# Optimization experiments

Measured on AMD Instinct MI355X. Metric: run time of the kernel, lower is better.

## Reference

```python
import jax, jax.numpy as jnp
import numpy as np

N, E = 25000, 400000
S, V, L2, T = 64, 32, 16, 64
NRBF, HID = 16, 128
ESD = NRBF + 16 + 20 + 8 + S + S + T     # 252 edge scalar dim
WDIM = 3 * S + 6 * V + 3 * L2            # 432 TP path weights
D = S + 6 * V + 5 * L2                   # 336 node irreps dim
FILM = 2 * S + 2 * V + L2                # 208 AdaLN modulation dim
CUTOFF = 5.0

def _basis():
    # orthonormal basis of symmetric traceless 3x3 matrices (l=2 Cartesian rep)
    r2, r6 = 1.0 / np.sqrt(2.0), 1.0 / np.sqrt(6.0)
    B = np.zeros((5, 3, 3), np.float32)
    B[0, 0, 1] = B[0, 1, 0] = r2
    B[1, 0, 2] = B[1, 2, 0] = r2
    B[2, 1, 2] = B[2, 2, 1] = r2
    B[3, 0, 0] = r2; B[3, 1, 1] = -r2
    B[4, 0, 0] = B[4, 1, 1] = r6; B[4, 2, 2] = -2.0 * r6
    return jnp.asarray(B)
B5 = _basis()

def rbf_encode(d, n_rbf):
    mu = jnp.linspace(0.0, CUTOFF, n_rbf)
    delta = CUTOFF / (n_rbf - 1)
    return jnp.exp(-(((d[:, None] - mu) / delta) ** 2))

def _model(h, coords, edge_ref_dist, t_emb,
           edge_type_emb, bond_type_emb, bond_conj_emb, bond_ring_emb, bond_stereo_emb,
           ref_W, ref_b, mlp_W1, mlp_b1, mlp_W2, mlp_b2,
           Wvs, Wls, Wsv, Wlv, Wvl, Wsl, P0, P1o, P1e, P2, film_W, film_b,
           edge_index, edge_type, edge_bond_type, edge_bond_conjugated,
           edge_bond_in_ring, edge_bond_stereo):
    src, dst = edge_index[0], edge_index[1]
    diff = coords[dst] - coords[src]
    dist = jnp.sqrt(jnp.sum(diff * diff, -1) + 1e-12)
    y1 = diff / dist[:, None]                                  # unit vector (Y1)
    y2 = jnp.einsum('kij,ei,ej->ek', B5, y1, y1)               # l=2 SH components
    # edge scalar features
    e_type = edge_type_emb[edge_type]
    is_bond = edge_bond_type >= 0
    conj_idx = jnp.where(is_bond, edge_bond_conjugated, 2)
    ring_idx = jnp.where(is_bond, edge_bond_in_ring, 2)
    e_bond = jnp.concatenate([bond_type_emb[edge_bond_type + 1], bond_conj_emb[conj_idx],
                              bond_ring_emb[ring_idx], bond_stereo_emb[edge_bond_stereo + 1]], -1)
    has_ref = (edge_ref_dist > 0).astype(h.dtype)
    dd = dist - edge_ref_dist
    e_ref = jnp.stack([jnp.abs(dd), dd, has_ref], -1) @ ref_W + ref_b
    h0 = h[:, :S]
    h1o = h[:, S:S + 3 * V].reshape(N, V, 3)
    h1e = h[:, S + 3 * V:S + 6 * V].reshape(N, V, 3)
    h2 = h[:, S + 6 * V:].reshape(N, L2, 5)
    es = jnp.concatenate([rbf_encode(dist, NRBF), e_type, e_bond, e_ref,
                          h0[src], h0[dst], t_emb[dst]], -1)   # [E, ESD]
    # edge MLP -> per-path depthwise TP weights
    w = jax.nn.silu(es @ mlp_W1 + mlp_b1) @ mlp_W2 + mlp_b2    # [E, WDIM]
    w00, w10, w20 = w[:, :S], w[:, S:2 * S], w[:, 2 * S:3 * S]
    o = 3 * S
    w11o = w[:, o:o + V]; w01o = w[:, o + V:o + 2 * V]
    wx1o = w[:, o + 2 * V:o + 3 * V]; w21o = w[:, o + 3 * V:o + 4 * V]
    w11e = w[:, o + 4 * V:o + 5 * V]; wx1e = w[:, o + 5 * V:o + 6 * V]
    o += 6 * V
    w22 = w[:, o:o + L2]; w112 = w[:, o + L2:o + 2 * L2]; w02 = w[:, o + 2 * L2:]
    h0s, h1os, h1es, h2s = h0[src], h1o[src], h1e[src], h2[src]
    By = jnp.einsum('kij,ej->eki', B5, y1)                     # [E,5,3]
    # 0e outputs: 0e*Y0, (1o.Y1), (2e.Y2)
    m0 = (w00 * h0s
          + w10 * (jnp.einsum('evi,ei->ev', h1os, y1) @ Wvs)
          + w20 * (jnp.einsum('eck,ek->ec', h2s, y2) @ Wls))
    # 1o outputs: 1o*Y0, 0e*Y1, 1e x Y1, 2e.Y1
    m1o = (w11o[..., None] * h1os
           + w01o[..., None] * ((h0s @ Wsv)[..., None] * y1[:, None, :])
           + wx1o[..., None] * jnp.cross(h1es, y1[:, None, :])
           + w21o[..., None] * jnp.einsum('eci,cv->evi', jnp.einsum('eck,eki->eci', h2s, By), Wlv))
    # 1e outputs: 1e*Y0, 1o x Y1
    m1e = w11e[..., None] * h1es + wx1e[..., None] * jnp.cross(h1os, y1[:, None, :])
    # 2e outputs: 2e*Y0, sym-traceless(1o outer Y1), 0e*Y2
    t112 = jnp.einsum('evi,eki->evk', h1os, By)                # projection onto B5
    m2 = (w22[..., None] * h2s
          + w112[..., None] * jnp.einsum('evk,vl->elk', t112, Wvl)
          + w02[..., None] * ((h0s @ Wsl)[..., None] * y2[:, None, :]))
    msg = jnp.concatenate([m0, m1o.reshape(E, -1), m1e.reshape(E, -1), m2.reshape(E, -1)], -1)
    agg = jax.ops.segment_sum(msg, dst, num_segments=N)        # scatter-aggregate
    # irrep-wise linear projection
    a0 = agg[:, :S] @ P0
    a1o = jnp.einsum('nvi,vw->nwi', agg[:, S:S + 3 * V].reshape(N, V, 3), P1o)
    a1e = jnp.einsum('nvi,vw->nwi', agg[:, S + 3 * V:S + 6 * V].reshape(N, V, 3), P1e)
    a2 = jnp.einsum('nck,cd->ndk', agg[:, S + 6 * V:].reshape(N, L2, 5), P2)
    a0 = jax.nn.silu(a0)                                       # scalar-only activation
    hn0 = h0 + a0
    hn1o = h1o + a1o
    hn1e = h1e + a1e
    hn2 = h2 + a2
    # equivariant AdaLN conditioned on t_emb
    film = t_emb @ film_W + film_b
    sc_s, sh_s = film[:, :S], film[:, S:2 * S]
    g1o = film[:, 2 * S:2 * S + V]; g1e = film[:, 2 * S + V:2 * S + 2 * V]; g2 = film[:, 2 * S + 2 * V:]
    mu = jnp.mean(hn0, -1, keepdims=True)
    var = jnp.var(hn0, -1, keepdims=True)
    hn0 = (hn0 - mu) / jnp.sqrt(var + 1e-6) * (1.0 + sc_s) + sh_s
    def vnorm(x, g):
        rms = jnp.sqrt(jnp.mean(jnp.sum(x * x, -1), -1, keepdims=True) + 1e-6)
        return x / rms[..., None] * (1.0 + g)[..., None]
    hn1o = vnorm(hn1o, g1o); hn1e = vnorm(hn1e, g1e); hn2 = vnorm(hn2, g2)
    return jnp.concatenate([hn0, hn1o.reshape(N, -1), hn1e.reshape(N, -1), hn2.reshape(N, -1)], -1)

def setup_inputs():
    key = jax.random.key(0)
    ks = iter(jax.random.split(key, 40))
    def nrm(shape, scale=None):
        s = scale if scale is not None else 1.0 / np.sqrt(shape[0])
        return jax.random.normal(next(ks), shape, jnp.float32) * s
    inp = {}
    inp['h'] = jax.random.normal(next(ks), (N, D), jnp.float32)
    inp['coords'] = jax.random.normal(next(ks), (N, 3), jnp.float32) * 3.0
    inp['edge_index'] = jax.random.randint(next(ks), (2, E), 0, N)
    inp['edge_type'] = jax.random.randint(next(ks), (E,), 0, 10)
    inp['edge_bond_type'] = jax.random.randint(next(ks), (E,), -1, 5)
    inp['edge_bond_conjugated'] = jax.random.randint(next(ks), (E,), 0, 2)
    inp['edge_bond_in_ring'] = jax.random.randint(next(ks), (E,), 0, 2)
    inp['edge_bond_stereo'] = jax.random.randint(next(ks), (E,), -1, 4)
    inp['edge_ref_dist'] = jax.random.uniform(next(ks), (E,), jnp.float32, 0.0, 2.0)
    inp['t_emb'] = jax.random.normal(next(ks), (N, T), jnp.float32)
    inp['edge_type_emb'] = nrm((10, 16), 0.5)
    inp['bond_type_emb'] = nrm((6, 8), 0.5)
    inp['bond_conj_emb'] = nrm((3, 4), 0.5)
    inp['bond_ring_emb'] = nrm((3, 4), 0.5)
    inp['bond_stereo_emb'] = nrm((5, 4), 0.5)
    inp['ref_W'] = nrm((3, 8)); inp['ref_b'] = jnp.zeros((8,), jnp.float32)
    inp['mlp_W1'] = nrm((ESD, HID)); inp['mlp_b1'] = jnp.zeros((HID,), jnp.float32)
    inp['mlp_W2'] = nrm((HID, WDIM)); inp['mlp_b2'] = jnp.zeros((WDIM,), jnp.float32)
    inp['Wvs'] = nrm((V, S)); inp['Wls'] = nrm((L2, S)); inp['Wsv'] = nrm((S, V))
    inp['Wlv'] = nrm((L2, V)); inp['Wvl'] = nrm((V, L2)); inp['Wsl'] = nrm((S, L2))
    inp['P0'] = nrm((S, S)); inp['P1o'] = nrm((V, V)); inp['P1e'] = nrm((V, V)); inp['P2'] = nrm((L2, L2))
    inp['film_W'] = nrm((T, FILM), 0.02); inp['film_b'] = jnp.zeros((FILM,), jnp.float32)
    return inp

def reference(h, coords, edge_index, edge_type, edge_bond_type, edge_bond_conjugated,
              edge_bond_in_ring, edge_bond_stereo, edge_ref_dist, t_emb,
              edge_type_emb, bond_type_emb, bond_conj_emb, bond_ring_emb, bond_stereo_emb,
              ref_W, ref_b, mlp_W1, mlp_b1, mlp_W2, mlp_b2,
              Wvs, Wls, Wsv, Wlv, Wvl, Wsl, P0, P1o, P1e, P2, film_W, film_b):
    return _model(h, coords, edge_ref_dist, t_emb,
                  edge_type_emb, bond_type_emb, bond_conj_emb, bond_ring_emb, bond_stereo_emb,
                  ref_W, ref_b, mlp_W1, mlp_b1, mlp_W2, mlp_b2,
                  Wvs, Wls, Wsv, Wlv, Wvl, Wsl, P0, P1o, P1e, P2, film_W, film_b,
                  edge_index, edge_type, edge_bond_type, edge_bond_conjugated,
                  edge_bond_in_ring, edge_bond_stereo)
```

## Files before the change

kernel.cpp:

```cpp
#include <hip/hip_runtime.h>
#include <hip/hip_bf16.h>

#define N_NODES 25000
#define N_EDGES 400000
#define S 64
#define V 32
#define L2C 16
#define TDIM 64
#define D 336
#define FILMD 208

#define ES_STR 264
#define HID_STR 136

#define PRE_STR 1152

typedef short bf8 __attribute__((ext_vector_type(8)));
typedef float f4  __attribute__((ext_vector_type(4)));
typedef unsigned int u32;
typedef u32 u32x2 __attribute__((ext_vector_type(2)));
typedef u32 u32x4 __attribute__((ext_vector_type(4)));

__device__ __forceinline__ float silu_f(float x) { return x / (1.0f + __expf(-x)); }

__device__ __forceinline__ float rl_f(float v, int lane) {
    return __int_as_float(__builtin_amdgcn_readlane(__float_as_int(v), lane));
}
__device__ __forceinline__ int rl_i(int v, int lane) {
    return __builtin_amdgcn_readlane(v, lane);
}

__device__ __forceinline__ float blo(u32 u) { return __uint_as_float(u << 16); }
__device__ __forceinline__ float bhi(u32 u) { return __uint_as_float(u & 0xffff0000u); }
__device__ __forceinline__ float bs(unsigned short u) { return __uint_as_float(((u32)u) << 16); }

__device__ __forceinline__ unsigned short f2b(float x) {
    union { __hip_bfloat16 b; unsigned short s; } c;
    c.b = __float2bfloat16(x);
    return c.s;
}
__device__ __forceinline__ u32 pk(float a, float b) {
    return (u32)f2b(a) | ((u32)f2b(b) << 16);
}

__device__ __forceinline__ float wsum64(float x) {
    #pragma unroll
    for (int m = 32; m > 0; m >>= 1) x += __shfl_xor(x, m, 64);
    return x;
}
__device__ __forceinline__ float wsum32(float x) {
    #pragma unroll
    for (int m = 16; m > 0; m >>= 1) x += __shfl_xor(x, m, 32);
    return x;
}
__device__ __forceinline__ float wsum16(float x) {
    #pragma unroll
    for (int m = 8; m > 0; m >>= 1) x += __shfl_xor(x, m, 16);
    return x;
}

__global__ __launch_bounds__(256) void convert_weights(
    const float* __restrict__ W1, const float* __restrict__ W2,
    __hip_bfloat16* __restrict__ Wb1t, __hip_bfloat16* __restrict__ Wb2t)
{
    const int i = blockIdx.x * 256 + threadIdx.x;
    if (i < 128 * 256) {
        const int n = i >> 8, k = i & 255;
        const float v = (k < 252) ? W1[k * 128 + n] : 0.0f;
        Wb1t[i] = __float2bfloat16(v);
    }
    if (i < 432 * 128) {
        const int n = i >> 7, k = i & 127;
        Wb2t[i] = __float2bfloat16(W2[k * 432 + n]);
    }
}

__global__ __launch_bounds__(256) void pre_kernel(
    const float* __restrict__ h,
    const float* __restrict__ Wvs, const float* __restrict__ Wls,
    const float* __restrict__ Wlv, const float* __restrict__ Wvl,
    const float* __restrict__ Wsv, const float* __restrict__ Wsl,
    unsigned short* __restrict__ pre)
{
    const int t = blockIdx.x * 256 + threadIdx.x;
    const int NA = N_NODES * 64;
    const int NC = N_NODES * 32;
    const int ND = N_NODES * 16;

    if (t < NA) {
        const int n = t >> 6, s = t & 63;
        const float* hn = h + (size_t)n * D;
        float g3x = 0.f, g3y = 0.f, g3z = 0.f;
        #pragma unroll 8
        for (int v = 0; v < 32; v++) {
            const float w = Wvs[v * 64 + s];
            g3x = fmaf(w, hn[64 + 3 * v], g3x);
            g3y = fmaf(w, hn[65 + 3 * v], g3y);
            g3z = fmaf(w, hn[66 + 3 * v], g3z);
        }
        float g40 = 0.f, g41 = 0.f, g42 = 0.f, g43 = 0.f, g44 = 0.f;
        #pragma unroll 4
        for (int c = 0; c < 16; c++) {
            const float w = Wls[c * 64 + s];
            g40 = fmaf(w, hn[256 + 5 * c], g40);
            g41 = fmaf(w, hn[257 + 5 * c], g41);
            g42 = fmaf(w, hn[258 + 5 * c], g42);
            g43 = fmaf(w, hn[259 + 5 * c], g43);
            g44 = fmaf(w, hn[260 + 5 * c], g44);
        }
        unsigned short* pr = pre + (size_t)n * PRE_STR;
        u32x4 oA = {pk(hn[s], g3x), pk(g3y, g3z), pk(g40, g41), pk(g42, g43)};
        *(u32x4*)(pr + s * 8) = oA;
        pr[512 + s] = f2b(g44);
    } else if (t < NA + NC) {
        const int u = t - NA;
        const int n = u >> 5, v = u & 31;
        const float* hn = h + (size_t)n * D;
        float g20 = 0.f, g21 = 0.f, g22 = 0.f, g23 = 0.f, g24 = 0.f;
        #pragma unroll 4
        for (int c = 0; c < 16; c++) {
            const float w = Wlv[c * 32 + v];
            g20 = fmaf(w, hn[256 + 5 * c], g20);
            g21 = fmaf(w, hn[257 + 5 * c], g21);
            g22 = fmaf(w, hn[258 + 5 * c], g22);
            g23 = fmaf(w, hn[259 + 5 * c], g23);
            g24 = fmaf(w, hn[260 + 5 * c], g24);
        }
        float pxv = 0.f;
        #pragma unroll 8
        for (int j = 0; j < 64; j++) pxv = fmaf(hn[j], Wsv[j * 32 + v], pxv);
        unsigned short* pr = pre + (size_t)n * PRE_STR + 576 + v * 12;
        u32x2 o0 = {pk(hn[64 + 3 * v], hn[65 + 3 * v]), pk(hn[66 + 3 * v], hn[160 + 3 * v])};
        u32x2 o1 = {pk(hn[161 + 3 * v], hn[162 + 3 * v]), pk(g20, g21)};
        u32x2 o2 = {pk(g22, g23), pk(g24, pxv)};
        *(u32x2*)(pr)     = o0;
        *(u32x2*)(pr + 4) = o1;
        *(u32x2*)(pr + 8) = o2;
    } else if (t < NA + NC + ND) {
        const int u = t - NA - NC;
        const int n = u >> 4, c = u & 15;
        const float* hn = h + (size_t)n * D;
        float g1x = 0.f, g1y = 0.f, g1z = 0.f;
        #pragma unroll 8
        for (int v = 0; v < 32; v++) {
            const float w = Wvl[v * 16 + c];
            g1x = fmaf(w, hn[64 + 3 * v], g1x);
            g1y = fmaf(w, hn[65 + 3 * v], g1y);
            g1z = fmaf(w, hn[66 + 3 * v], g1z);
        }
        float pxl = 0.f;
        #pragma unroll 8
        for (int j = 0; j < 64; j++) pxl = fmaf(hn[j], Wsl[j * 16 + c], pxl);
        unsigned short* pr = pre + (size_t)n * PRE_STR + 960 + c * 12;
        u32x2 o0 = {pk(hn[256 + 5 * c], hn[257 + 5 * c]), pk(hn[258 + 5 * c], hn[259 + 5 * c])};
        u32x2 o1 = {pk(hn[260 + 5 * c], g1x), pk(g1y, g1z)};
        u32x2 o2 = {pk(pxl, 0.f), pk(0.f, 0.f)};
        *(u32x2*)(pr)     = o0;
        *(u32x2*)(pr + 4) = o1;
        *(u32x2*)(pr + 8) = o2;
    }
}

__global__ __launch_bounds__(256) void film_kernel(
    const float* __restrict__ t_emb, const float* __restrict__ filmW,
    const float* __restrict__ filmb, unsigned short* __restrict__ flm)
{
    const int n = blockIdx.x * 4 + (threadIdx.x >> 6);
    const int l = threadIdx.x & 63;
    if (n >= N_NODES) return;
    const float* tr = t_emb + (size_t)n * TDIM;
    const int c2 = 128 + l, c3 = 192 + (l & 15);
    float f0 = filmb[l], f1 = filmb[64 + l], f2 = filmb[c2], f3 = filmb[c3];
    #pragma unroll 4
    for (int t = 0; t < 64; t++) {
        const float tt = tr[t];
        const float* fr = filmW + t * FILMD;
        f0 = fmaf(tt, fr[l], f0);
        f1 = fmaf(tt, fr[64 + l], f1);
        f2 = fmaf(tt, fr[c2], f2);
        f3 = fmaf(tt, fr[c3], f3);
    }
    u32x2 o = {pk(f0, f1), pk(f2, f3)};
    *(u32x2*)(flm + (size_t)n * 256 + l * 4) = o;
}

__global__ __launch_bounds__(256) void hist_kernel(const int* __restrict__ eidx, int* __restrict__ cnt) {
    const int e = blockIdx.x * 256 + threadIdx.x;
    if (e < N_EDGES) atomicAdd(&cnt[eidx[N_EDGES + e]], 1);
}

__global__ __launch_bounds__(1024) void scan_kernel(const int* __restrict__ cnt, int* __restrict__ offs) {
    __shared__ int part[1024];
    const int t = threadIdx.x;
    const int base = t * 25;
    int s = 0;
    for (int k = 0; k < 25; k++) {
        const int b = base + k;
        s += (b < N_NODES) ? cnt[b] : 0;
    }
    part[t] = s;
    __syncthreads();
    for (int off = 1; off < 1024; off <<= 1) {
        int v = (t >= off) ? part[t - off] : 0;
        __syncthreads();
        part[t] += v;
        __syncthreads();
    }
    int run = (t > 0) ? part[t - 1] : 0;
    for (int k = 0; k < 25; k++) {
        const int b = base + k;
        if (b < N_NODES) { offs[b] = run; run += cnt[b]; }
    }
    if (t == 1023) offs[N_NODES] = part[1023];
}

__global__ __launch_bounds__(256) void scatter_sort_kernel(
    const int* __restrict__ eidx, const int* __restrict__ offs,
    int* __restrict__ cur, int* __restrict__ sorted,
    int* __restrict__ ssrc, int* __restrict__ sdst)
{
    const int e = blockIdx.x * 256 + threadIdx.x;
    if (e < N_EDGES) {
        const int s = eidx[e];
        const int d = eidx[N_EDGES + e];
        const int p = offs[d] + atomicAdd(&cur[d], 1);
        if (p >= 0 && p < N_EDGES) { sorted[p] = e; ssrc[p] = s; sdst[p] = d; }
    }
}

__global__ __launch_bounds__(256, 3) void mlp_chunk(
    const float* __restrict__ h, const float* __restrict__ coords,
    const int* __restrict__ sorted, const int* __restrict__ ssrc,
    const int* __restrict__ sdst,
    const int* __restrict__ offs, int n_lo, int n_hi,
    const int* __restrict__ etype, const int* __restrict__ ebt,
    const int* __restrict__ econj, const int* __restrict__ ering,
    const int* __restrict__ est, const float* __restrict__ eref,
    const float* __restrict__ t_emb,
    const float* __restrict__ type_emb, const float* __restrict__ bt_emb,
    const float* __restrict__ conj_emb, const float* __restrict__ ring_emb,
    const float* __restrict__ st_emb,
    const float* __restrict__ refW, const float* __restrict__ refb,
    const __hip_bfloat16* __restrict__ Wb1t, const float* __restrict__ b1,
    const __hip_bfloat16* __restrict__ Wb2t, const float* __restrict__ b2,
    __hip_bfloat16* __restrict__ w_buf)
{
    __shared__ __hip_bfloat16 esA[64 * ES_STR];
    __shared__ __hip_bfloat16 hidA[64 * HID_STR];

    const int wid = threadIdx.x >> 6;
    const int l   = threadIdx.x & 63;
    const int pbase = offs[n_lo];
    const int pend  = offs[n_hi];
    const int start = pbase + blockIdx.x * 64;
    if (start >= pend) return;

    {
        const int myp = min(start + l, pend - 1);
        const int e_l   = sorted[myp];
        const int src_l = ssrc[myp];
        const int dst_l = sdst[myp];
        const int et_l = etype[e_l];
        const int bt_l = ebt[e_l];
        const int cj_l = econj[e_l];
        const int rg_l = ering[e_l];
        const int st_l = est[e_l];
        const float er_l = eref[e_l];
        const float csx_l = coords[3 * src_l], csy_l = coords[3 * src_l + 1], csz_l = coords[3 * src_l + 2];
        const float cdx_l = coords[3 * dst_l], cdy_l = coords[3 * dst_l + 1], cdz_l = coords[3 * dst_l + 2];

        for (int i = 0; i < 16; i++) {
            const int le = wid * 16 + i;
            const int src = rl_i(src_l, le);
            const int dst = rl_i(dst_l, le);
            const float dx = rl_f(cdx_l, le) - rl_f(csx_l, le);
            const float dy = rl_f(cdy_l, le) - rl_f(csy_l, le);
            const float dz = rl_f(cdz_l, le) - rl_f(csz_l, le);
            const float dist = sqrtf(dx * dx + dy * dy + dz * dz + 1e-12f);
            __hip_bfloat16* es = esA + le * ES_STR;
            es[60 + l]  = __float2bfloat16(h[(size_t)src * D + l]);
            es[124 + l] = __float2bfloat16(h[(size_t)dst * D + l]);
            es[188 + l] = __float2bfloat16(t_emb[(size_t)dst * TDIM + l]);
            const int et = rl_i(et_l, le);
            const int bt = rl_i(bt_l, le);
            const int ci = (bt >= 0) ? rl_i(cj_l, le) : 2;
            const int ri = (bt >= 0) ? rl_i(rg_l, le) : 2;
            const int si = rl_i(st_l, le) + 1;
            const float er = rl_f(er_l, le);
            if (l < 16) {
                const float mu = (float)l * (5.0f / 15.0f);
                const float t = (dist - mu) * 3.0f;
                es[l] = __float2bfloat16(__expf(-t * t));
                es[16 + l] = __float2bfloat16(type_emb[et * 16 + l]);
            }
            if (l < 8) {
                es[32 + l] = __float2bfloat16(bt_emb[(bt + 1) * 8 + l]);
                const float ddv = dist - er;
                const float hr = (er > 0.f) ? 1.f : 0.f;
                es[52 + l] = __float2bfloat16(
                    fabsf(ddv) * refW[l] + ddv * refW[8 + l] + hr * refW[16 + l] + refb[l]);
            }
            if (l < 4) {
                es[40 + l] = __float2bfloat16(conj_emb[ci * 4 + l]);
                es[44 + l] = __float2bfloat16(ring_emb[ri * 4 + l]);
                es[48 + l] = __float2bfloat16(st_emb[si * 4 + l]);
                es[252 + l] = __float2bfloat16(0.0f);
            }
        }
    }
    __syncthreads();

    {
        const int q = l >> 4;
        const int t16 = l & 15;
        f4 acc[4][2];
        #pragma unroll
        for (int mt = 0; mt < 4; mt++)
            #pragma unroll
            for (int nt = 0; nt < 2; nt++) acc[mt][nt] = (f4){0.f, 0.f, 0.f, 0.f};
        const int n0 = wid * 32 + t16;
        #pragma unroll
        for (int kk = 0; kk < 256; kk += 32) {
            const int k0 = kk + q * 8;
            bf8 a[4];
            #pragma unroll
            for (int mt = 0; mt < 4; mt++)
                a[mt] = *(const bf8*)(esA + (mt * 16 + t16) * ES_STR + k0);
            bf8 b[2];
            b[0] = *(const bf8*)(Wb1t + (size_t)n0 * 256 + k0);
            b[1] = *(const bf8*)(Wb1t + (size_t)(n0 + 16) * 256 + k0);
            #pragma unroll
            for (int mt = 0; mt < 4; mt++) {
                acc[mt][0] = __builtin_amdgcn_mfma_f32_16x16x32_bf16(a[mt], b[0], acc[mt][0], 0, 0, 0);
                acc[mt][1] = __builtin_amdgcn_mfma_f32_16x16x32_bf16(a[mt], b[1], acc[mt][1], 0, 0, 0);
            }
        }
        const float bias0 = b1[n0], bias1 = b1[n0 + 16];
        #pragma unroll
        for (int mt = 0; mt < 4; mt++) {
            #pragma unroll
            for (int r = 0; r < 4; r++) {
                const int m = mt * 16 + q * 4 + r;
                hidA[m * HID_STR + n0]      = __float2bfloat16(silu_f(acc[mt][0][r] + bias0));
                hidA[m * HID_STR + n0 + 16] = __float2bfloat16(silu_f(acc[mt][1][r] + bias1));
            }
        }
    }
    __syncthreads();

    {
        const int q = l >> 4;
        const int t16 = l & 15;
        bf8 a2[4][4];
        #pragma unroll
        for (int ks = 0; ks < 4; ks++) {
            const int k0 = ks * 32 + q * 8;
            #pragma unroll
            for (int mt = 0; mt < 4; mt++)
                a2[mt][ks] = *(const bf8*)(hidA + (mt * 16 + t16) * HID_STR + k0);
        }
        const size_t wb = (size_t)(start - pbase);
        for (int t = wid; t < 27; t += 4) {
            const int n = t * 16 + t16;
            f4 acc[4];
            #pragma unroll
            for (int mt = 0; mt < 4; mt++) acc[mt] = (f4){0.f, 0.f, 0.f, 0.f};
            #pragma unroll
            for (int ks = 0; ks < 4; ks++) {
                const bf8 b = *(const bf8*)(Wb2t + (size_t)n * 128 + ks * 32 + q * 8);
                #pragma unroll
                for (int mt = 0; mt < 4; mt++)
                    acc[mt] = __builtin_amdgcn_mfma_f32_16x16x32_bf16(a2[mt][ks], b, acc[mt], 0, 0, 0);
            }
            const float bias = b2[n];
            #pragma unroll
            for (int mt = 0; mt < 4; mt++) {
                #pragma unroll
                for (int r = 0; r < 4; r++) {
                    const int m = mt * 16 + q * 4 + r;
                    w_buf[(wb + m) * 432 + n] = __float2bfloat16(acc[mt][r] + bias);
                }
            }
        }
    }
}


#define EDECL(E) u32x4 E##_A; unsigned short E##_g44; u32x2 E##_Ea, E##_Eb, E##_Ec; \
    unsigned short E##_w0, E##_w1, E##_w2, E##_wa, E##_wb, E##_wc, E##_w6, E##_w7, E##_w8;

#define PRE_LD(E, ii) { \
    const int src_ = rl_i(bsrc_l, (ii)); \
    const unsigned short* pr_ = pre + (size_t)src_ * PRE_STR; \
    const unsigned short* wr_ = wbase + (size_t)(ii) * 432; \
    E##_A   = *(const u32x4*)(pr_ + l * 8); \
    E##_g44 = pr_[512 + l]; \
    E##_Ea  = *(const u32x2*)(pr_ + rbase); \
    E##_Eb  = *(const u32x2*)(pr_ + rbase + 4); \
    E##_Ec  = *(const u32x2*)(pr_ + rbase + 8); \
    E##_w0 = __builtin_nontemporal_load(wr_ + l); \
    E##_w1 = __builtin_nontemporal_load(wr_ + 64 + l); \
    E##_w2 = __builtin_nontemporal_load(wr_ + 128 + l); \
    E##_wa = __builtin_nontemporal_load(wr_ + wb0); \
    E##_wb = __builtin_nontemporal_load(wr_ + wb1); \
    E##_wc = __builtin_nontemporal_load(wr_ + wb2); \
    E##_w6 = __builtin_nontemporal_load(wr_ + wb3); \
    E##_w7 = __builtin_nontemporal_load(wr_ + wb4); \
    E##_w8 = __builtin_nontemporal_load(wr_ + wb5); \
}

#define ECOMP(E, ii) { \
    const float dx = cdx - rl_f(bcsx, (ii)); \
    const float dy = cdy - rl_f(bcsy, (ii)); \
    const float dz = cdz - rl_f(bcsz, (ii)); \
    const float dist = sqrtf(dx * dx + dy * dy + dz * dz + 1e-12f); \
    const float inv = 1.0f / dist; \
    const float ux = dx * inv, uy = dy * inv, uz = dz * inv; \
    const float y20 = 2.f * R2 * ux * uy; \
    const float y21 = 2.f * R2 * ux * uz; \
    const float y22 = 2.f * R2 * uy * uz; \
    const float y23 = R2 * (ux * ux - uy * uy); \
    const float y24 = R6 * (ux * ux + uy * uy - 2.f * uz * uz); \
    const float rx2 = R2 * ux, ry2 = R2 * uy, rz2 = R2 * uz; \
    const float rx6 = R6 * ux, ry6 = R6 * uy, rz6 = -2.f * R6 * uz; \
    const float w0 = bs(E##_w0), w1 = bs(E##_w1), w2 = bs(E##_w2); \
    const float wa = bs(E##_wa), wbv = bs(E##_wb), wc = bs(E##_wc); \
    { \
        const float h0  = blo(E##_A.x), g3x = bhi(E##_A.x); \
        const float g3y = blo(E##_A.y), g3z = bhi(E##_A.y); \
        const float g40 = blo(E##_A.z), g41 = bhi(E##_A.z); \
        const float g42 = blo(E##_A.w), g43 = bhi(E##_A.w); \
        const float g44 = bs(E##_g44); \
        const float t1 = g3x * ux + g3y * uy + g3z * uz; \
        const float t2 = g40 * y20 + g41 * y21 + g42 * y22 + g43 * y23 + g44 * y24; \
        am0 += w0 * h0 + w1 * t1 + w2 * t2; \
    } \
    if (loV) { \
        const float a0 = blo(E##_Ea.x), a1 = bhi(E##_Ea.x), a2 = blo(E##_Ea.y); \
        const float b0 = bhi(E##_Ea.y), b1 = blo(E##_Eb.x), b2 = bhi(E##_Eb.x); \
        const float g20 = blo(E##_Eb.y), g21 = bhi(E##_Eb.y); \
        const float g22 = blo(E##_Ec.x), g23 = bhi(E##_Ec.x); \
        const float g24 = blo(E##_Ec.y), pxv = bhi(E##_Ec.y); \
        const float w6 = bs(E##_w6), w7 = bs(E##_w7), w8 = bs(E##_w8); \
        const float t0v = g20 * ry2 + g21 * rz2 + g23 * rx2 + g24 * rx6; \
        const float t1v = g20 * rx2 + g22 * rz2 - g23 * ry2 + g24 * ry6; \
        const float t2v = g21 * rx2 + g22 * ry2 + g24 * rz6; \
        const float co0 = b1 * uz - b2 * uy; \
        const float co1 = b2 * ux - b0 * uz; \
        const float co2 = b0 * uy - b1 * ux; \
        const float ce0 = a1 * uz - a2 * uy; \
        const float ce1 = a2 * ux - a0 * uz; \
        const float ce2 = a0 * uy - a1 * ux; \
        const float pv = wbv * pxv; \
        am1[0] += wa * a0 + pv * ux + wc * co0 + w6 * t0v; \
        am1[1] += wa * a1 + pv * uy + wc * co1 + w6 * t1v; \
        am1[2] += wa * a2 + pv * uz + wc * co2 + w6 * t2v; \
        am1[3] += w7 * b0 + w8 * ce0; \
        am1[4] += w7 * b1 + w8 * ce1; \
        am1[5] += w7 * b2 + w8 * ce2; \
    } else { \
        const float c0 = blo(E##_Ea.x), c1 = bhi(E##_Ea.x), c2 = blo(E##_Ea.y), c3 = bhi(E##_Ea.y); \
        const float c4 = blo(E##_Eb.x), g1x = bhi(E##_Eb.x), g1y = blo(E##_Eb.y), g1z = bhi(E##_Eb.y); \
        const float pxl = blo(E##_Ec.x); \
        const float tl0 = g1x * ry2 + g1y * rx2; \
        const float tl1 = g1x * rz2 + g1z * rx2; \
        const float tl2 = g1y * rz2 + g1z * ry2; \
        const float tl3 = g1x * rx2 - g1y * ry2; \
        const float tl4 = g1x * rx6 + g1y * ry6 + g1z * rz6; \
        const float pl = wc * pxl; \
        am2[0] += wa * c0 + wbv * tl0 + pl * y20; \
        am2[1] += wa * c1 + wbv * tl1 + pl * y21; \
        am2[2] += wa * c2 + wbv * tl2 + pl * y22; \
        am2[3] += wa * c3 + wbv * tl3 + pl * y23; \
        am2[4] += wa * c4 + wbv * tl4 + pl * y24; \
    } \
}

__global__ __launch_bounds__(256, 4) void gather_chunk(
    const float* __restrict__ h, const float* __restrict__ coords,
    const int* __restrict__ ssrc,
    const int* __restrict__ offs, int n_lo, int n_hi,
    const __hip_bfloat16* __restrict__ w_buf,
    const unsigned short* __restrict__ pre, const unsigned short* __restrict__ flm,
    const float* __restrict__ P0, const float* __restrict__ P1o,
    const float* __restrict__ P1e, const float* __restrict__ P2,
    float* __restrict__ out)
{
    __shared__ float agL[4][344];
    __shared__ float sP0[64 * 64];
    __shared__ float sP1o[32 * 32];
    __shared__ float sP1e[32 * 32];
    __shared__ float sP2[16 * 16];

    const int wid = threadIdx.x >> 6;
    const int l   = threadIdx.x & 63;
    const int tid = threadIdx.x;

    #pragma unroll 4
    for (int j = tid; j < 4096; j += 256) sP0[j] = P0[j];
    #pragma unroll 4
    for (int j = tid; j < 1024; j += 256) { sP1o[j] = P1o[j]; sP1e[j] = P1e[j]; }
    sP2[tid] = P2[tid];
    __syncthreads();

    const int n = n_lo + blockIdx.x * 4 + wid;
    if (n >= n_hi) return;

    float* ag = agL[wid];

    const float R2 = 0.7071067811865476f;
    const float R6 = 0.4082482904638631f;

    const int pbase = offs[n_lo];
    const int vv = l & 31, cc = l & 15;
    const bool loV = (l < 32);
    const bool hiA = (l >= 32) && !(l & 16);

    const int rbase = loV ? (576 + vv * 12) : (960 + cc * 12);
    const int wb0 = loV ? (192 + vv) : (384 + cc);
    const int wb1 = loV ? (224 + vv) : (400 + cc);
    const int wb2 = loV ? (256 + vv) : (416 + cc);
    const int wb3 = loV ? (288 + vv) : wb0;
    const int wb4 = loV ? (320 + vv) : wb1;
    const int wb5 = loV ? (352 + vv) : wb2;

    const float cdx = coords[3 * n], cdy = coords[3 * n + 1], cdz = coords[3 * n + 2];
    const int pbeg = offs[n], pend = offs[n + 1];

    float am0 = 0.f;
    float am1[6] = {0.f, 0.f, 0.f, 0.f, 0.f, 0.f};
    float am2[5] = {0.f, 0.f, 0.f, 0.f, 0.f};

    for (int pb = pbeg; pb < pend; pb += 64) {
        const int tail = pend - pb;
        const int bcnt = tail < 64 ? tail : 64;
        const int bpos = pb + (l < tail ? l : tail - 1);
        const int bsrc_l = ssrc[bpos];
        const float bcsx = coords[3 * bsrc_l];
        const float bcsy = coords[3 * bsrc_l + 1];
        const float bcsz = coords[3 * bsrc_l + 2];
        const unsigned short* wbase = (const unsigned short*)w_buf + (size_t)(pb - pbase) * 432;

        for (int i = 0; i < bcnt; i += 2) {
            EDECL(e0); EDECL(e1);
            PRE_LD(e0, i);
            const bool has2 = (i + 1 < bcnt);
            if (has2) PRE_LD(e1, i + 1);
            ECOMP(e0, i);
            if (has2) ECOMP(e1, i + 1);
        }
    }

    ag[l] = am0;
    if (loV) {
        ag[64 + 3 * l + 0] = am1[0];
        ag[64 + 3 * l + 1] = am1[1];
        ag[64 + 3 * l + 2] = am1[2];
        ag[160 + 3 * l + 0] = am1[3];
        ag[160 + 3 * l + 1] = am1[4];
        ag[160 + 3 * l + 2] = am1[5];
    }
    if (hiA) {
        #pragma unroll
        for (int k = 0; k < 5; k++) ag[256 + 5 * cc + k] = am2[k];
    }

    const float* hrow = h + (size_t)n * D;

    const u32x2 F = *(const u32x2*)(flm + (size_t)n * 256 + l * 4);
    const float f0 = blo(F.x), f1 = bhi(F.x), f2 = blo(F.y), f3 = bhi(F.y);

    {
        float a0 = 0.f;
        #pragma unroll 8
        for (int j = 0; j < 64; j++) a0 = fmaf(ag[j], sP0[j * 64 + l], a0);
        a0 = silu_f(a0);
        const float hn0 = hrow[l] + a0;
        const float mu = wsum64(hn0) * (1.0f / 64.0f);
        const float d0 = hn0 - mu;
        const float var = wsum64(d0 * d0) * (1.0f / 64.0f);
        out[(size_t)n * D + l] = d0 * rsqrtf(var + 1e-6f) * (1.f + f0) + f1;
    }

    {
        const int v = l & 31;
        const bool iso = (l < 32);
        const float* Pm = iso ? sP1o : sP1e;
        const int base = iso ? 64 : 160;
        float a0 = 0.f, a1 = 0.f, a2 = 0.f;
        #pragma unroll 8
        for (int u = 0; u < 32; u++) {
            const float p = Pm[u * 32 + v];
            a0 = fmaf(ag[base + 3 * u + 0], p, a0);
            a1 = fmaf(ag[base + 3 * u + 1], p, a1);
            a2 = fmaf(ag[base + 3 * u + 2], p, a2);
        }
        const float x0 = hrow[base + 3 * v + 0] + a0;
        const float x1 = hrow[base + 3 * v + 1] + a1;
        const float x2 = hrow[base + 3 * v + 2] + a2;
        const float ssq = x0 * x0 + x1 * x1 + x2 * x2;
        const float s = wsum32(ssq);
        const float rinv = rsqrtf(s * (1.f / 32.f) + 1e-6f);
        const float scv = (1.f + f2) * rinv;
        out[(size_t)n * D + base + 3 * v + 0] = x0 * scv;
        out[(size_t)n * D + base + 3 * v + 1] = x1 * scv;
        out[(size_t)n * D + base + 3 * v + 2] = x2 * scv;
    }

    {
        const int c = l & 15;
        float xk[5];
        float ssq = 0.f;
        #pragma unroll
        for (int k = 0; k < 5; k++) {
            float a = 0.f;
            #pragma unroll
            for (int u = 0; u < 16; u++) a = fmaf(ag[256 + 5 * u + k], sP2[u * 16 + c], a);
            const float x = hrow[256 + 5 * c + k] + a;
            xk[k] = x;
            ssq += x * x;
        }
        const float s = wsum16(ssq);
        const float rinv = rsqrtf(s * (1.f / 16.f) + 1e-6f);
        const float scv = (1.f + f3) * rinv;
        if (l < 16) {
            #pragma unroll
            for (int k = 0; k < 5; k++) out[(size_t)n * D + 256 + 5 * c + k] = xk[k] * scv;
        }
    }
}

extern "C" void kernel_launch(void* const* d_in, const int* in_sizes, int n_in,
                              void* d_out, int out_size, void* d_ws, size_t ws_size,
                              hipStream_t stream)
{
    const float* h        = (const float*)d_in[0];
    const float* coords   = (const float*)d_in[1];
    const int*   eidx     = (const int*)d_in[2];
    const int*   etype    = (const int*)d_in[3];
    const int*   ebt      = (const int*)d_in[4];
    const int*   econj    = (const int*)d_in[5];
    const int*   ering    = (const int*)d_in[6];
    const int*   est      = (const int*)d_in[7];
    const float* eref     = (const float*)d_in[8];
    const float* t_emb    = (const float*)d_in[9];
    const float* type_emb = (const float*)d_in[10];
    const float* bt_emb   = (const float*)d_in[11];
    const float* conj_emb = (const float*)d_in[12];
    const float* ring_emb = (const float*)d_in[13];
    const float* st_emb   = (const float*)d_in[14];
    const float* refW     = (const float*)d_in[15];
    const float* refb     = (const float*)d_in[16];
    const float* W1       = (const float*)d_in[17];
    const float* b1       = (const float*)d_in[18];
    const float* W2       = (const float*)d_in[19];
    const float* b2       = (const float*)d_in[20];
    const float* Wvs      = (const float*)d_in[21];
    const float* Wls      = (const float*)d_in[22];
    const float* Wsv      = (const float*)d_in[23];
    const float* Wlv      = (const float*)d_in[24];
    const float* Wvl      = (const float*)d_in[25];
    const float* Wsl      = (const float*)d_in[26];
    const float* P0       = (const float*)d_in[27];
    const float* P1o      = (const float*)d_in[28];
    const float* P1e      = (const float*)d_in[29];
    const float* P2       = (const float*)d_in[30];
    const float* filmW    = (const float*)d_in[31];
    const float* filmb    = (const float*)d_in[32];

    float* out = (float*)d_out;

    char* base = (char*)d_ws;
    size_t off = 0;
    auto alloc = [&](size_t bytes, size_t align) -> char* {
        off = (off + align - 1) / align * align;
        char* p = base + off;
        off += bytes;
        return p;
    };
    int* cnt = (int*)alloc((size_t)(2 * N_NODES + N_NODES + 1 + 3 * N_EDGES) * sizeof(int), 256);
    int* cur    = cnt + N_NODES;
    int* offs   = cur + N_NODES;
    int* sorted = offs + N_NODES + 1;
    int* ssrc   = sorted + N_EDGES;
    int* sdst   = ssrc + N_EDGES;
    unsigned short* pre = (unsigned short*)alloc((size_t)N_NODES * PRE_STR * sizeof(unsigned short), 256);
    unsigned short* flm = (unsigned short*)alloc((size_t)N_NODES * 256 * sizeof(unsigned short), 256);
    __hip_bfloat16* Wb1t = (__hip_bfloat16*)alloc(128 * 256 * 2, 256);
    __hip_bfloat16* Wb2t = (__hip_bfloat16*)alloc(432 * 128 * 2, 256);
    off = (off + 255) / 256 * 256;
    __hip_bfloat16* w_buf = (__hip_bfloat16*)(base + off);
    size_t rem = (ws_size > off) ? (ws_size - off) : 0;

    long cap_edges = (long)(rem / (432 * 2));
    int EBLK = (int)(cap_edges / 64);
    if (EBLK > (N_EDGES + 63) / 64) EBLK = (N_EDGES + 63) / 64;
    if (EBLK < 1) EBLK = 1;
    int NCH, nchunks;
    if ((long)EBLK * 64 >= N_EDGES) {
        NCH = N_NODES; nchunks = 1;
    } else {
        NCH = (int)((long)EBLK * 64 / 21);
        if (NCH < 1) NCH = 1;
        nchunks = (N_NODES + NCH - 1) / NCH;
    }

    hipMemsetAsync(cnt, 0, 2 * N_NODES * sizeof(int), stream);

    convert_weights<<<(432 * 128 + 255) / 256, 256, 0, stream>>>(W1, W2, Wb1t, Wb2t);
    {
        const int tot = N_NODES * (64 + 32 + 16);
        pre_kernel<<<(tot + 255) / 256, 256, 0, stream>>>(h, Wvs, Wls, Wlv, Wvl, Wsv, Wsl, pre);
    }
    film_kernel<<<(N_NODES + 3) / 4, 256, 0, stream>>>(t_emb, filmW, filmb, flm);
    hist_kernel<<<(N_EDGES + 255) / 256, 256, 0, stream>>>(eidx, cnt);
    scan_kernel<<<1, 1024, 0, stream>>>(cnt, offs);
    scatter_sort_kernel<<<(N_EDGES + 255) / 256, 256, 0, stream>>>(eidx, offs, cur, sorted, ssrc, sdst);

    for (int k = 0; k < nchunks; k++) {
        const int n_lo = k * NCH;
        int n_hi = n_lo + NCH;
        if (n_hi > N_NODES) n_hi = N_NODES;

        mlp_chunk<<<EBLK, 256, 0, stream>>>(
            h, coords, sorted, ssrc, sdst, offs, n_lo, n_hi,
            etype, ebt, econj, ering, est, eref, t_emb,
            type_emb, bt_emb, conj_emb, ring_emb, st_emb, refW, refb,
            Wb1t, b1, Wb2t, b2, w_buf);

        const int nn = n_hi - n_lo;
        const int nb = (nn + 3) / 4;
        gather_chunk<<<nb, 256, 0, stream>>>(
            h, coords, ssrc, offs, n_lo, n_hi, w_buf, pre, flm,
            P0, P1o, P1e, P2, out);
    }
}
```

Before: 1.018 ms.

## Pre-convert node features to bf16 and rebuild edge-feature staging with vector stores

```diff
diff --git a/kernel.cpp b/kernel.cpp
--- a/kernel.cpp
+++ b/kernel.cpp
@@ -66,7 +66,10 @@
     const int i = blockIdx.x * 256 + threadIdx.x;
     if (i < 128 * 256) {
         const int n = i >> 8, k = i & 255;
-        const float v = (k < 252) ? W1[k * 128 + n] : 0.0f;
+        float v;
+        if (k < 60) v = W1[k * 128 + n];
+        else if (k < 64) v = 0.0f;
+        else v = W1[(k - 4) * 128 + n];
         Wb1t[i] = __float2bfloat16(v);
     }
     if (i < 432 * 128) {
@@ -162,8 +165,10 @@
 }
 
 __global__ __launch_bounds__(256) void film_kernel(
+    const float* __restrict__ h,
     const float* __restrict__ t_emb, const float* __restrict__ filmW,
-    const float* __restrict__ filmb, unsigned short* __restrict__ flm)
+    const float* __restrict__ filmb, unsigned short* __restrict__ flm,
+    unsigned short* __restrict__ h0b, unsigned short* __restrict__ tb)
 {
     const int n = blockIdx.x * 4 + (threadIdx.x >> 6);
     const int l = threadIdx.x & 63;
@@ -182,6 +187,8 @@
     }
     u32x2 o = {pk(f0, f1), pk(f2, f3)};
     *(u32x2*)(flm + (size_t)n * 256 + l * 4) = o;
+    h0b[(size_t)n * 64 + l] = f2b(h[(size_t)n * D + l]);
+    tb[(size_t)n * 64 + l]  = f2b(tr[l]);
 }
 
 __global__ __launch_bounds__(256) void hist_kernel(const int* __restrict__ eidx, int* __restrict__ cnt) {
@@ -229,18 +236,19 @@
 }
 
 __global__ __launch_bounds__(256, 3) void mlp_chunk(
-    const float* __restrict__ h, const float* __restrict__ coords,
+    const float* __restrict__ coords,
     const int* __restrict__ sorted, const int* __restrict__ ssrc,
     const int* __restrict__ sdst,
     const int* __restrict__ offs, int n_lo, int n_hi,
     const int* __restrict__ etype, const int* __restrict__ ebt,
     const int* __restrict__ econj, const int* __restrict__ ering,
     const int* __restrict__ est, const float* __restrict__ eref,
-    const float* __restrict__ t_emb,
+    const int* __restrict__ unused0,
     const float* __restrict__ type_emb, const float* __restrict__ bt_emb,
     const float* __restrict__ conj_emb, const float* __restrict__ ring_emb,
     const float* __restrict__ st_emb,
     const float* __restrict__ refW, const float* __restrict__ refb,
+    const unsigned short* __restrict__ h0b, const unsigned short* __restrict__ tb,
     const __hip_bfloat16* __restrict__ Wb1t, const float* __restrict__ b1,
     const __hip_bfloat16* __restrict__ Wb2t, const float* __restrict__ b2,
     __hip_bfloat16* __restrict__ w_buf)
@@ -256,56 +264,77 @@
     if (start >= pend) return;
 
     {
-        const int myp = min(start + l, pend - 1);
-        const int e_l   = sorted[myp];
-        const int src_l = ssrc[myp];
-        const int dst_l = sdst[myp];
-        const int et_l = etype[e_l];
-        const int bt_l = ebt[e_l];
-        const int cj_l = econj[e_l];
-        const int rg_l = ering[e_l];
-        const int st_l = est[e_l];
-        const float er_l = eref[e_l];
-        const float csx_l = coords[3 * src_l], csy_l = coords[3 * src_l + 1], csz_l = coords[3 * src_l + 2];
-        const float cdx_l = coords[3 * dst_l], cdy_l = coords[3 * dst_l + 1], cdz_l = coords[3 * dst_l + 2];
-
-        for (int i = 0; i < 16; i++) {
-            const int le = wid * 16 + i;
-            const int src = rl_i(src_l, le);
-            const int dst = rl_i(dst_l, le);
-            const float dx = rl_f(cdx_l, le) - rl_f(csx_l, le);
-            const float dy = rl_f(cdy_l, le) - rl_f(csy_l, le);
-            const float dz = rl_f(cdz_l, le) - rl_f(csz_l, le);
-            const float dist = sqrtf(dx * dx + dy * dy + dz * dz + 1e-12f);
-            __hip_bfloat16* es = esA + le * ES_STR;
-            es[60 + l]  = __float2bfloat16(h[(size_t)src * D + l]);
-            es[124 + l] = __float2bfloat16(h[(size_t)dst * D + l]);
-            es[188 + l] = __float2bfloat16(t_emb[(size_t)dst * TDIM + l]);
-            const int et = rl_i(et_l, le);
-            const int bt = rl_i(bt_l, le);
-            const int ci = (bt >= 0) ? rl_i(cj_l, le) : 2;
-            const int ri = (bt >= 0) ? rl_i(rg_l, le) : 2;
-            const int si = rl_i(st_l, le) + 1;
-            const float er = rl_f(er_l, le);
-            if (l < 16) {
-                const float mu = (float)l * (5.0f / 15.0f);
-                const float t = (dist - mu) * 3.0f;
-                es[l] = __float2bfloat16(__expf(-t * t));
-                es[16 + l] = __float2bfloat16(type_emb[et * 16 + l]);
+        u32* es32 = (u32*)esA;
+        const int le  = wid * 16 + (l >> 2);
+        const int q   = l & 3;
+        const int myp = min(start + le, pend - 1);
+        const int e   = sorted[myp];
+        const int src = ssrc[myp];
+        const int dst = sdst[myp];
+        const float dx = coords[3 * dst]     - coords[3 * src];
+        const float dy = coords[3 * dst + 1] - coords[3 * src + 1];
+        const float dz = coords[3 * dst + 2] - coords[3 * src + 2];
+        const float dist = sqrtf(dx * dx + dy * dy + dz * dz + 1e-12f);
+
+        u32 ow[8];
+        if (q == 0) {
+            #pragma unroll
+            for (int j = 0; j < 8; j++) {
+                const float m0 = (float)(2 * j) * (1.0f / 3.0f);
+                const float m1 = (float)(2 * j + 1) * (1.0f / 3.0f);
+                const float t0 = (dist - m0) * 3.0f;
+                const float t1 = (dist - m1) * 3.0f;
+                ow[j] = pk(__expf(-t0 * t0), __expf(-t1 * t1));
             }
-            if (l < 8) {
-                es[32 + l] = __float2bfloat16(bt_emb[(bt + 1) * 8 + l]);
-                const float ddv = dist - er;
-                const float hr = (er > 0.f) ? 1.f : 0.f;
-                es[52 + l] = __float2bfloat16(
-                    fabsf(ddv) * refW[l] + ddv * refW[8 + l] + hr * refW[16 + l] + refb[l]);
-            }
-            if (l < 4) {
-                es[40 + l] = __float2bfloat16(conj_emb[ci * 4 + l]);
-                es[44 + l] = __float2bfloat16(ring_emb[ri * 4 + l]);
-                es[48 + l] = __float2bfloat16(st_emb[si * 4 + l]);
-                es[252 + l] = __float2bfloat16(0.0f);
-            }
+        } else if (q == 1) {
+            const float* te = type_emb + etype[e] * 16;
+            #pragma unroll
+            for (int j = 0; j < 8; j++) ow[j] = pk(te[2 * j], te[2 * j + 1]);
+        } else if (q == 2) {
+            const int bt = ebt[e];
+            const int ci = (bt >= 0) ? econj[e] : 2;
+            const int ri = (bt >= 0) ? ering[e] : 2;
+            const float* bb = bt_emb + (bt + 1) * 8;
+            ow[0] = pk(bb[0], bb[1]); ow[1] = pk(bb[2], bb[3]);
+            ow[2] = pk(bb[4], bb[5]); ow[3] = pk(bb[6], bb[7]);
+            const float* cj = conj_emb + ci * 4;
+            ow[4] = pk(cj[0], cj[1]); ow[5] = pk(cj[2], cj[3]);
+            const float* rg = ring_emb + ri * 4;
+            ow[6] = pk(rg[0], rg[1]); ow[7] = pk(rg[2], rg[3]);
+        } else {
+            const float* se = st_emb + (est[e] + 1) * 4;
+            ow[0] = pk(se[0], se[1]); ow[1] = pk(se[2], se[3]);
+            const float er = eref[e];
+            const float ddv = dist - er;
+            const float hr = (er > 0.f) ? 1.f : 0.f;
+            const float ad = fabsf(ddv);
+            float rf[8];
+            #pragma unroll
+            for (int j = 0; j < 8; j++)
+                rf[j] = ad * refW[j] + ddv * refW[8 + j] + hr * refW[16 + j] + refb[j];
+            ow[2] = pk(rf[0], rf[1]); ow[3] = pk(rf[2], rf[3]);
+            ow[4] = pk(rf[4], rf[5]); ow[5] = pk(rf[6], rf[7]);
+            ow[6] = 0u; ow[7] = 0u;
+        }
+        u32* er = es32 + le * (ES_STR / 2) + q * 8;
+        *(u32x4*)(er)     = (u32x4){ow[0], ow[1], ow[2], ow[3]};
+        *(u32x4*)(er + 4) = (u32x4){ow[4], ow[5], ow[6], ow[7]};
+    }
+    {
+        u32* es32 = (u32*)esA;
+        const u32* h32 = (const u32*)h0b;
+        const u32* t32 = (const u32*)tb;
+        const int rr = l >> 5, w16 = l & 31;
+        #pragma unroll
+        for (int j = 0; j < 8; j++) {
+            const int le2 = wid * 16 + 2 * j + rr;
+            const int myp2 = min(start + le2, pend - 1);
+            const int s2 = ssrc[myp2];
+            const int d2 = sdst[myp2];
+            u32* er = es32 + le2 * (ES_STR / 2);
+            er[32 + w16] = h32[(size_t)s2 * 32 + w16];
+            er[64 + w16] = h32[(size_t)d2 * 32 + w16];
+            er[96 + w16] = t32[(size_t)d2 * 32 + w16];
         }
     }
     __syncthreads();
@@ -686,6 +715,8 @@
     int* sdst   = ssrc + N_EDGES;
     unsigned short* pre = (unsigned short*)alloc((size_t)N_NODES * PRE_STR * sizeof(unsigned short), 256);
     unsigned short* flm = (unsigned short*)alloc((size_t)N_NODES * 256 * sizeof(unsigned short), 256);
+    unsigned short* h0b = (unsigned short*)alloc((size_t)N_NODES * 64 * sizeof(unsigned short), 256);
+    unsigned short* tb  = (unsigned short*)alloc((size_t)N_NODES * 64 * sizeof(unsigned short), 256);
     __hip_bfloat16* Wb1t = (__hip_bfloat16*)alloc(128 * 256 * 2, 256);
     __hip_bfloat16* Wb2t = (__hip_bfloat16*)alloc(432 * 128 * 2, 256);
     off = (off + 255) / 256 * 256;
@@ -700,7 +731,7 @@
     if ((long)EBLK * 64 >= N_EDGES) {
         NCH = N_NODES; nchunks = 1;
     } else {
-        NCH = (int)((long)EBLK * 64 / 21);
+        NCH = (int)((long)EBLK * 64 / 18);
         if (NCH < 1) NCH = 1;
         nchunks = (N_NODES + NCH - 1) / NCH;
     }
@@ -712,7 +743,7 @@
         const int tot = N_NODES * (64 + 32 + 16);
         pre_kernel<<<(tot + 255) / 256, 256, 0, stream>>>(h, Wvs, Wls, Wlv, Wvl, Wsv, Wsl, pre);
     }
-    film_kernel<<<(N_NODES + 3) / 4, 256, 0, stream>>>(t_emb, filmW, filmb, flm);
+    film_kernel<<<(N_NODES + 3) / 4, 256, 0, stream>>>(h, t_emb, filmW, filmb, flm, h0b, tb);
     hist_kernel<<<(N_EDGES + 255) / 256, 256, 0, stream>>>(eidx, cnt);
     scan_kernel<<<1, 1024, 0, stream>>>(cnt, offs);
     scatter_sort_kernel<<<(N_EDGES + 255) / 256, 256, 0, stream>>>(eidx, offs, cur, sorted, ssrc, sdst);
@@ -723,10 +754,10 @@
         if (n_hi > N_NODES) n_hi = N_NODES;
 
         mlp_chunk<<<EBLK, 256, 0, stream>>>(
-            h, coords, sorted, ssrc, sdst, offs, n_lo, n_hi,
-            etype, ebt, econj, ering, est, eref, t_emb,
+            coords, sorted, ssrc, sdst, offs, n_lo, n_hi,
+            etype, ebt, econj, ering, est, eref, (const int*)nullptr,
             type_emb, bt_emb, conj_emb, ring_emb, st_emb, refW, refb,
-            Wb1t, b1, Wb2t, b2, w_buf);
+            h0b, tb, Wb1t, b1, Wb2t, b2, w_buf);
 
         const int nn = n_hi - n_lo;
         const int nb = (nn + 3) / 4;
```

Measured after the change: 853.6 us. -16.1%, faster.
